# Kernel tuning notes

Measured on AMD Instinct MI355X. Metric: run time of the kernel, lower is better.

## Reference

```python
import jax, jax.numpy as jnp
import numpy as np

B, L, H, E = 4, 2048, 8, 64
S, D = L, E  # causal mask forces L == S


def setup_inputs() -> dict:
    key = jax.random.key(0)
    kq, kk, kv, km = jax.random.split(key, 4)
    return {
        "queries": jax.random.normal(kq, (B, L, H, E), dtype=jnp.float32),
        "keys": jax.random.normal(kk, (B, S, H, E), dtype=jnp.float32),
        "values": jax.random.normal(kv, (B, S, H, D), dtype=jnp.float32),
        "map": jax.random.normal(km, (S, S), dtype=jnp.float32),
    }


def reference(queries, keys, values, map):
    # queries: [B,L,H,E], keys: [B,S,H,E], values: [B,S,H,D], map: [S,S]
    E_ = queries.shape[-1]
    scale = 1.0 / jnp.sqrt(jnp.asarray(E_, dtype=queries.dtype))
    # raw attention scores: [B,H,L,S]
    scores = jnp.einsum("blhe,bshe->bhls", queries, keys)
    # mix scores with learned map along the key axis: [B,H,L,S]
    scores = jnp.einsum("bhls,st->bhlt", scores, map)
    # causal mask (TriangularCausalMask: triu with diagonal=1 is masked)
    Lq = queries.shape[1]
    causal = jnp.triu(jnp.ones((Lq, Lq), dtype=bool), k=1)  # [L,S]
    scores = jnp.where(causal[None, None, :, :], -jnp.inf, scores)
    attn = jax.nn.softmax(scale * scores, axis=-1)  # dropout p=0.0 -> identity
    out = jnp.einsum("bhls,bshd->blhd", attn, values)  # [B,L,H,D]
    return out
```

## Files before the change

kernel.cpp:

```cpp
#include <hip/hip_runtime.h>


typedef short bf16x8 __attribute__((ext_vector_type(8)));
typedef float f32x4 __attribute__((ext_vector_type(4)));
typedef float f32x16 __attribute__((ext_vector_type(16)));
typedef unsigned short u16x8 __attribute__((ext_vector_type(8)));
typedef unsigned int u32x4 __attribute__((ext_vector_type(4)));

typedef __attribute__((address_space(1))) const void gvoid;
typedef __attribute__((address_space(3))) void lvoid;

__device__ __forceinline__ unsigned short f2bf(float x) {
  unsigned int u = __float_as_uint(x);
  u += 0x7FFFu + ((u >> 16) & 1u);
  return (unsigned short)(u >> 16);
}
__device__ __forceinline__ float bf2f(unsigned short h) {
  return __uint_as_float(((unsigned int)h) << 16);
}
__device__ __forceinline__ unsigned int cvtpk(float lo, float hi) {
  unsigned int r;
  asm("v_cvt_pk_bf16_f32 %0, %1, %2" : "=v"(r) : "v"(lo), "v"(hi));
  return r;
}

__device__ __forceinline__ void gload16(const unsigned short* g, unsigned short* l) {
  __builtin_amdgcn_global_load_lds((gvoid*)g, (lvoid*)l, 16, 0, 0);
}

template <int NW>
__device__ __forceinline__ void stage_tile(const unsigned short* __restrict__ g,
                                           int gstride, unsigned short* l,
                                           int rows, int tid) {
  const int lane = tid & 63, w = tid >> 6;
  const int nch = rows << 3;
  for (int c0 = (w << 6); c0 < nch; c0 += NW * 64) {
    const int c = c0 + lane;
    const int row = c >> 3;
    const int bir = (c & 7) << 4;
    const int sb = bir ^ ((row & 7) << 4);
    gload16(g + (size_t)row * gstride + (sb >> 1), l + (size_t)c0 * 8);
  }
}

__device__ __forceinline__ int swz(int row, int byteInRow) {
  return row * 128 + (byteInRow ^ ((row & 7) << 4));
}

__global__ __launch_bounds__(256) void prep_m(const float* __restrict__ M,
                                              unsigned short* __restrict__ Mh,
                                              unsigned short* __restrict__ Ml) {
  __shared__ float Ts[64][68];
  const int s0 = blockIdx.x << 6, t0 = blockIdx.y << 6;
  const int tid = threadIdx.x, r = tid >> 2, c0 = (tid & 3) << 4;
  const float* src = M + (size_t)(s0 + r) * 2048 + t0 + c0;
#pragma unroll
  for (int j = 0; j < 4; ++j)
    *(float4*)&Ts[r][c0 + 4 * j] = *(const float4*)(src + 4 * j);
  __syncthreads();
  u16x8 h0, h1, l0v, l1v;
#pragma unroll
  for (int j = 0; j < 8; ++j) {
    float x = Ts[c0 + j][r];
    unsigned short hh = f2bf(x);
    h0[j] = hh; l0v[j] = f2bf(x - bf2f(hh));
  }
#pragma unroll
  for (int j = 8; j < 16; ++j) {
    float x = Ts[c0 + j][r];
    unsigned short hh = f2bf(x);
    h1[j - 8] = hh; l1v[j - 8] = f2bf(x - bf2f(hh));
  }
  const size_t o = (size_t)(t0 + r) * 2048 + s0 + c0;
  *(u16x8*)(Mh + o) = h0; *(u16x8*)(Mh + o + 8) = h1;
  *(u16x8*)(Ml + o) = l0v; *(u16x8*)(Ml + o + 8) = l1v;
}

__global__ __launch_bounds__(256) void prep_kv(const float* __restrict__ src4d,
                                               unsigned short* __restrict__ Dh,
                                               unsigned short* __restrict__ Dl,
                                               int has_lo) {
  __shared__ float Ts[64][68];
  const int s0 = blockIdx.x << 6, bh = blockIdx.y;
  const int b = bh >> 3, h = bh & 7;
  const int tid = threadIdx.x, r = tid >> 2, c0 = (tid & 3) << 4;
  const float* src = src4d + ((size_t)(b * 2048 + s0 + r) * 8 + h) * 64 + c0;
#pragma unroll
  for (int j = 0; j < 4; ++j)
    *(float4*)&Ts[r][c0 + 4 * j] = *(const float4*)(src + 4 * j);
  __syncthreads();
  u16x8 h0, h1, l0v, l1v;
#pragma unroll
  for (int j = 0; j < 8; ++j) {
    float x = Ts[c0 + j][r];
    unsigned short hh = f2bf(x);
    h0[j] = hh; l0v[j] = f2bf(x - bf2f(hh));
  }
#pragma unroll
  for (int j = 8; j < 16; ++j) {
    float x = Ts[c0 + j][r];
    unsigned short hh = f2bf(x);
    h1[j - 8] = hh; l1v[j - 8] = f2bf(x - bf2f(hh));
  }
  const size_t o = ((size_t)bh * 64 + r) * 2048 + s0 + c0;
  *(u16x8*)(Dh + o) = h0; *(u16x8*)(Dh + o + 8) = h1;
  if (has_lo) { *(u16x8*)(Dl + o) = l0v; *(u16x8*)(Dl + o + 8) = l1v; }
}

__global__ __launch_bounds__(512, 2) void km_mfma2(
    const unsigned short* __restrict__ Mth, const unsigned short* __restrict__ Mtl,
    const unsigned short* __restrict__ Kth, const unsigned short* __restrict__ Ktl,
    unsigned short* __restrict__ KMh, unsigned short* __restrict__ KMl) {
  __shared__ __attribute__((aligned(16))) unsigned short sm[40960];
  unsigned short* MH = sm;
  unsigned short* ML = sm + 16384;
  unsigned short* KH = sm + 32768;
  unsigned short* KL = sm + 36864;
  const int tid = threadIdx.x, lane = tid & 63, w = tid >> 6;
  const int g2 = lane >> 5, li5 = lane & 31;
  const int tc = w & 3, sh = w >> 2;

  const int x = (int)blockIdx.x & 7;
  const int bh = (int)blockIdx.x >> 3;
  const int t0 = x << 8;

  const unsigned short* MthB = Mth + (size_t)t0 * 2048;
  const unsigned short* MtlB = Mtl + (size_t)t0 * 2048;
  const unsigned short* KthB = Kth + (size_t)bh * 64 * 2048;
  const unsigned short* KtlB = Ktl + (size_t)bh * 64 * 2048;

  f32x16 acc[2][2];
#pragma unroll
  for (int tf = 0; tf < 2; ++tf)
#pragma unroll
    for (int ef = 0; ef < 2; ++ef)
      acc[tf][ef] = (f32x16){0,0,0,0,0,0,0,0,0,0,0,0,0,0,0,0};

  for (int s0 = 0; s0 < 2048; s0 += 64) {
    __syncthreads();
    stage_tile<8>(MthB + s0, 2048, MH, 256, tid);
    stage_tile<8>(MtlB + s0, 2048, ML, 256, tid);
    stage_tile<8>(KthB + s0, 2048, KH, 64, tid);
    stage_tile<8>(KtlB + s0, 2048, KL, 64, tid);
    asm volatile("s_waitcnt vmcnt(0)" ::: "memory");
    __syncthreads();

    __builtin_amdgcn_s_setprio(1);
#pragma unroll
    for (int kg = 0; kg < 2; ++kg) {
      const int kb = ((sh << 1) + kg) * 32 + (g2 << 4);
      const int ra0 = (tc << 6) + li5;
      const bf16x8 aH0 = *(const bf16x8*)((const char*)MH + swz(ra0, kb));
      const bf16x8 aL0 = *(const bf16x8*)((const char*)ML + swz(ra0, kb));
      const bf16x8 aH1 = *(const bf16x8*)((const char*)MH + swz(ra0 + 32, kb));
      const bf16x8 aL1 = *(const bf16x8*)((const char*)ML + swz(ra0 + 32, kb));
      const bf16x8 bH0 = *(const bf16x8*)((const char*)KH + swz(li5, kb));
      const bf16x8 bL0 = *(const bf16x8*)((const char*)KL + swz(li5, kb));
      const bf16x8 bH1 = *(const bf16x8*)((const char*)KH + swz(32 + li5, kb));
      const bf16x8 bL1 = *(const bf16x8*)((const char*)KL + swz(32 + li5, kb));
      acc[0][0] = __builtin_amdgcn_mfma_f32_32x32x16_bf16(aH0, bH0, acc[0][0], 0, 0, 0);
      acc[0][0] = __builtin_amdgcn_mfma_f32_32x32x16_bf16(aH0, bL0, acc[0][0], 0, 0, 0);
      acc[0][0] = __builtin_amdgcn_mfma_f32_32x32x16_bf16(aL0, bH0, acc[0][0], 0, 0, 0);
      acc[0][1] = __builtin_amdgcn_mfma_f32_32x32x16_bf16(aH0, bH1, acc[0][1], 0, 0, 0);
      acc[0][1] = __builtin_amdgcn_mfma_f32_32x32x16_bf16(aH0, bL1, acc[0][1], 0, 0, 0);
      acc[0][1] = __builtin_amdgcn_mfma_f32_32x32x16_bf16(aL0, bH1, acc[0][1], 0, 0, 0);
      acc[1][0] = __builtin_amdgcn_mfma_f32_32x32x16_bf16(aH1, bH0, acc[1][0], 0, 0, 0);
      acc[1][0] = __builtin_amdgcn_mfma_f32_32x32x16_bf16(aH1, bL0, acc[1][0], 0, 0, 0);
      acc[1][0] = __builtin_amdgcn_mfma_f32_32x32x16_bf16(aL1, bH0, acc[1][0], 0, 0, 0);
      acc[1][1] = __builtin_amdgcn_mfma_f32_32x32x16_bf16(aH1, bH1, acc[1][1], 0, 0, 0);
      acc[1][1] = __builtin_amdgcn_mfma_f32_32x32x16_bf16(aH1, bL1, acc[1][1], 0, 0, 0);
      acc[1][1] = __builtin_amdgcn_mfma_f32_32x32x16_bf16(aL1, bH1, acc[1][1], 0, 0, 0);
    }
    __builtin_amdgcn_s_setprio(0);
  }

  __syncthreads();
  float* red = (float*)sm;
  if (sh == 1) {
#pragma unroll
    for (int tf = 0; tf < 2; ++tf)
#pragma unroll
      for (int ef = 0; ef < 2; ++ef) {
        const int fi = (tc << 2) | (tf << 1) | ef;
        float* dst = red + (size_t)(fi * 64 + lane) * 17;
#pragma unroll
        for (int rr = 0; rr < 16; ++rr) dst[rr] = acc[tf][ef][rr];
      }
  }
  __syncthreads();
  if (sh == 0) {
    const size_t base = (size_t)bh * (2048 * 64);
#pragma unroll
    for (int tf = 0; tf < 2; ++tf)
#pragma unroll
      for (int ef = 0; ef < 2; ++ef) {
        const int fi = (tc << 2) | (tf << 1) | ef;
        const float* src = red + (size_t)(fi * 64 + lane) * 17;
#pragma unroll
        for (int rr = 0; rr < 16; ++rr) {
          const float v = acc[tf][ef][rr] + src[rr];
          const int trow = t0 + (tc << 6) + (tf << 5) + (g2 << 2) +
                           ((rr >> 2) << 3) + (rr & 3);
          const int e = (ef << 5) + li5;
          const unsigned short hh = f2bf(v);
          const size_t idx = base + (size_t)trow * 64 + e;
          KMh[idx] = hh;
          KMl[idx] = f2bf(v - bf2f(hh));
        }
      }
  }
}

__global__ __launch_bounds__(256, 3) void attn32(
    const float* __restrict__ Q, const unsigned short* __restrict__ KMh,
    const unsigned short* __restrict__ KMl, const unsigned short* __restrict__ Vt,
    float* __restrict__ Out, float* __restrict__ Opart, float* __restrict__ Ml) {
  __shared__ __attribute__((aligned(16))) unsigned short sm[24576];
  const int tid = threadIdx.x, lane = tid & 63, w = tid >> 6;
  const int g2 = lane >> 5, li5 = lane & 31;

  const int bid = (int)blockIdx.x;
  const int x = bid & 7, n = bid >> 3;
  const int slot = n >> 5, j = n & 31;
  const int bh = (x << 2) | (j & 3);
  const int kk = j >> 2;
  int lt, jt0, jtEnd;
  bool partial;
  if (slot == 2) {
    lt = kk; jt0 = 0; jtEnd = 2 * kk + 1; partial = false;
  } else {
    lt = 15 - kk;
    const int half = 16 - kk;
    jt0 = slot * half; jtEnd = jt0 + half - 1; partial = true;
  }
  const int b = bh >> 3, h = bh & 7;
  const int l0 = lt << 7;
  const int qg = l0 + (w << 5) + li5;
  const int rloc = (w << 5) + li5;

  const float SC2 = 0.18033688011112042f;
  bf16x8 qh[4], ql[4];
  {
    const float* qsrc = Q + (((size_t)(b * 2048 + qg) * 8 + h) << 6) + (g2 << 3);
#pragma unroll
    for (int kki = 0; kki < 4; ++kki) {
      const float4 v0 = *(const float4*)(qsrc + 16 * kki);
      const float4 v1 = *(const float4*)(qsrc + 16 * kki + 4);
      const float xs[8] = {v0.x, v0.y, v0.z, v0.w, v1.x, v1.y, v1.z, v1.w};
#pragma unroll
      for (int jj = 0; jj < 8; ++jj) {
        const float xv = xs[jj] * SC2;
        const unsigned short hh = f2bf(xv);
        qh[kki][jj] = (short)hh;
        ql[kki][jj] = (short)f2bf(xv - bf2f(hh));
      }
    }
  }

  f32x16 o0 = {0,0,0,0,0,0,0,0,0,0,0,0,0,0,0,0};
  f32x16 o1 = {0,0,0,0,0,0,0,0,0,0,0,0,0,0,0,0};
  f32x16 lsacc = {0,0,0,0,0,0,0,0,0,0,0,0,0,0,0,0};
  float m2 = -1e30f;
  bf16x8 ones;
#pragma unroll
  for (int jj = 0; jj < 8; ++jj) ones[jj] = (short)0x3F80;

  const unsigned short* KHb = KMh + (size_t)bh * 2048 * 64;
  const unsigned short* KLb = KMl + (size_t)bh * 2048 * 64;
  const unsigned short* VTb = Vt + (size_t)bh * 64 * 2048;

  const int jtmax_w = 2 * lt + (w >> 1);

  {
    unsigned short* s0b = sm + (jt0 & 1) * 12288;
    stage_tile<4>(KHb + (size_t)jt0 * 4096, 64, s0b, 64, tid);
    stage_tile<4>(KLb + (size_t)jt0 * 4096, 64, s0b + 4096, 64, tid);
    stage_tile<4>(VTb + jt0 * 64, 2048, s0b + 8192, 64, tid);
  }
  asm volatile("s_waitcnt vmcnt(0)" ::: "memory");
  __builtin_amdgcn_s_barrier();
  __builtin_amdgcn_sched_barrier(0);

  for (int jt = jt0; jt <= jtEnd; ++jt) {
    const int cur = jt & 1;
    if (jt < jtEnd) {
      unsigned short* nb = sm + (cur ^ 1) * 12288;
      stage_tile<4>(KHb + (size_t)(jt + 1) * 4096, 64, nb, 64, tid);
      stage_tile<4>(KLb + (size_t)(jt + 1) * 4096, 64, nb + 4096, 64, tid);
      stage_tile<4>(VTb + (jt + 1) * 64, 2048, nb + 8192, 64, tid);
    }

    if (jt <= jtmax_w) {
      const unsigned short* KH = sm + cur * 12288;
      const unsigned short* KL = KH + 4096;
      const unsigned short* VT = KH + 8192;

      f32x16 z0 = {0,0,0,0,0,0,0,0,0,0,0,0,0,0,0,0};
      f32x16 z1 = {0,0,0,0,0,0,0,0,0,0,0,0,0,0,0,0};
      __builtin_amdgcn_s_setprio(1);
#pragma unroll
      for (int kki = 0; kki < 4; ++kki) {
        const int cb = 32 * kki + 16 * g2;
        const bf16x8 a0h = *(const bf16x8*)((const char*)KH + swz(li5, cb));
        const bf16x8 a0l = *(const bf16x8*)((const char*)KL + swz(li5, cb));
        const bf16x8 a1h = *(const bf16x8*)((const char*)KH + swz(32 + li5, cb));
        const bf16x8 a1l = *(const bf16x8*)((const char*)KL + swz(32 + li5, cb));
        z0 = __builtin_amdgcn_mfma_f32_32x32x16_bf16(a0h, qh[kki], z0, 0, 0, 0);
        z0 = __builtin_amdgcn_mfma_f32_32x32x16_bf16(a0h, ql[kki], z0, 0, 0, 0);
        z0 = __builtin_amdgcn_mfma_f32_32x32x16_bf16(a0l, qh[kki], z0, 0, 0, 0);
        z1 = __builtin_amdgcn_mfma_f32_32x32x16_bf16(a1h, qh[kki], z1, 0, 0, 0);
        z1 = __builtin_amdgcn_mfma_f32_32x32x16_bf16(a1h, ql[kki], z1, 0, 0, 0);
        z1 = __builtin_amdgcn_mfma_f32_32x32x16_bf16(a1l, qh[kki], z1, 0, 0, 0);
      }
      __builtin_amdgcn_s_setprio(0);

      const bool needmask = (jt * 64 + 63 > l0 + (w << 5));
      if (needmask) {
        const int thr = qg - jt * 64;
#pragma unroll
        for (int rr = 0; rr < 16; ++rr) {
          const int tl = (g2 << 2) + ((rr >> 2) << 3) + (rr & 3);
          if (tl > thr) z0[rr] = -1e30f;
          if (tl + 32 > thr) z1[rr] = -1e30f;
        }
      }

      float t16[16];
#pragma unroll
      for (int rr = 0; rr < 16; ++rr) t16[rr] = fmaxf(z0[rr], z1[rr]);
#pragma unroll
      for (int s = 8; s; s >>= 1)
#pragma unroll
        for (int rr = 0; rr < 8; ++rr)
          if (rr < s) t16[rr] = fmaxf(t16[rr], t16[rr + s]);
      const float mx = fmaxf(t16[0], __shfl_xor(t16[0], 32));
      if (__any(mx > m2 + 11.0f)) {
        const float m2n = fmaxf(m2, mx);
        const float fs = exp2f(m2 - m2n);
        m2 = m2n;
#pragma unroll
        for (int rr = 0; rr < 16; ++rr) { o0[rr] *= fs; o1[rr] *= fs; }
        lsacc[0] *= fs;
      }

      float pv0[16], pv1[16];
#pragma unroll
      for (int rr = 0; rr < 16; ++rr) {
        pv0[rr] = exp2f(z0[rr] - m2);
        pv1[rr] = exp2f(z1[rr] - m2);
      }
      unsigned int W0[8], W1[8];
#pragma unroll
      for (int i = 0; i < 8; ++i) {
        W0[i] = cvtpk(pv0[2 * i], pv0[2 * i + 1]);
        W1[i] = cvtpk(pv1[2 * i], pv1[2 * i + 1]);
      }
      asm volatile("v_permlane32_swap_b32 %0, %1" : "+v"(W0[0]), "+v"(W0[2]));
      asm volatile("v_permlane32_swap_b32 %0, %1" : "+v"(W0[1]), "+v"(W0[3]));
      asm volatile("v_permlane32_swap_b32 %0, %1" : "+v"(W0[4]), "+v"(W0[6]));
      asm volatile("v_permlane32_swap_b32 %0, %1" : "+v"(W0[5]), "+v"(W0[7]));
      asm volatile("v_permlane32_swap_b32 %0, %1" : "+v"(W1[0]), "+v"(W1[2]));
      asm volatile("v_permlane32_swap_b32 %0, %1" : "+v"(W1[1]), "+v"(W1[3]));
      asm volatile("v_permlane32_swap_b32 %0, %1" : "+v"(W1[4]), "+v"(W1[6]));
      asm volatile("v_permlane32_swap_b32 %0, %1" : "+v"(W1[5]), "+v"(W1[7]));
      bf16x8 pf[4];
      {
        u32x4 f0 = {W0[0], W0[1], W0[2], W0[3]};
        u32x4 f1 = {W0[4], W0[5], W0[6], W0[7]};
        u32x4 f2 = {W1[0], W1[1], W1[2], W1[3]};
        u32x4 f3 = {W1[4], W1[5], W1[6], W1[7]};
        pf[0] = __builtin_bit_cast(bf16x8, f0);
        pf[1] = __builtin_bit_cast(bf16x8, f1);
        pf[2] = __builtin_bit_cast(bf16x8, f2);
        pf[3] = __builtin_bit_cast(bf16x8, f3);
      }

      __builtin_amdgcn_s_setprio(1);
#pragma unroll
      for (int kki = 0; kki < 4; ++kki) {
        const int cb = 32 * kki + 16 * g2;
        const bf16x8 v0f = *(const bf16x8*)((const char*)VT + swz(li5, cb));
        const bf16x8 v1f = *(const bf16x8*)((const char*)VT + swz(32 + li5, cb));
        o0 = __builtin_amdgcn_mfma_f32_32x32x16_bf16(v0f, pf[kki], o0, 0, 0, 0);
        o1 = __builtin_amdgcn_mfma_f32_32x32x16_bf16(v1f, pf[kki], o1, 0, 0, 0);
        lsacc = __builtin_amdgcn_mfma_f32_32x32x16_bf16(ones, pf[kki], lsacc, 0, 0, 0);
      }
      __builtin_amdgcn_s_setprio(0);
    }

    asm volatile("s_waitcnt vmcnt(0)" ::: "memory");
    __builtin_amdgcn_s_barrier();
    __builtin_amdgcn_sched_barrier(0);
  }

  if (!partial) {
    const float inv = 1.f / lsacc[0];
    float* ob = Out + (((size_t)(b * 2048 + qg) * 8 + h) << 6);
#pragma unroll
    for (int r2 = 0; r2 < 4; ++r2) {
      const int doff = (g2 << 2) + (r2 << 3);
      float4 s0 = make_float4(o0[4 * r2] * inv, o0[4 * r2 + 1] * inv,
                              o0[4 * r2 + 2] * inv, o0[4 * r2 + 3] * inv);
      *(float4*)(ob + doff) = s0;
      float4 s1 = make_float4(o1[4 * r2] * inv, o1[4 * r2 + 1] * inv,
                              o1[4 * r2 + 2] * inv, o1[4 * r2 + 3] * inv);
      *(float4*)(ob + 32 + doff) = s1;
    }
  } else {
    const size_t pidx = (((size_t)slot * 32 + bh) * 8 + kk) * 128 + rloc;
    float* op = Opart + pidx * 64;
#pragma unroll
    for (int r2 = 0; r2 < 4; ++r2) {
      const int doff = (g2 << 2) + (r2 << 3);
      *(float4*)(op + doff) =
          make_float4(o0[4 * r2], o0[4 * r2 + 1], o0[4 * r2 + 2], o0[4 * r2 + 3]);
      *(float4*)(op + 32 + doff) =
          make_float4(o1[4 * r2], o1[4 * r2 + 1], o1[4 * r2 + 2], o1[4 * r2 + 3]);
    }
    Ml[pidx * 2] = m2;
    Ml[pidx * 2 + 1] = lsacc[0];
  }
}

__global__ __launch_bounds__(256) void attn_combine(
    const float* __restrict__ Opart, const float* __restrict__ Ml,
    float* __restrict__ Out) {
  const int tid = threadIdx.x;
  const int rowg = (int)blockIdx.x * 32 + (tid >> 3);
  const int d0 = (tid & 7) << 3;
  const int r = rowg & 127, kk = (rowg >> 7) & 7, bh = rowg >> 10;
  const int b = bh >> 3, h = bh & 7;
  const int lt = 15 - kk;
  const size_t pidx = (((size_t)bh * 8 + kk) * 128 + r);
  const size_t PSLOT = (size_t)32 * 8 * 128 * 64;
  const size_t MSLOT = (size_t)32 * 8 * 128 * 2;
  const float m0 = Ml[pidx * 2], ls0 = Ml[pidx * 2 + 1];
  const float m1 = Ml[MSLOT + pidx * 2], ls1 = Ml[MSLOT + pidx * 2 + 1];
  const float mm = fmaxf(m0, m1);
  const float w0 = exp2f(m0 - mm), w1 = exp2f(m1 - mm);
  const float inv = 1.f / (ls0 * w0 + ls1 * w1);
  const float* p0 = Opart + pidx * 64 + d0;
  const float* p1 = Opart + PSLOT + pidx * 64 + d0;
  const float4 a0 = *(const float4*)(p0);
  const float4 a1 = *(const float4*)(p0 + 4);
  const float4 b0 = *(const float4*)(p1);
  const float4 b1 = *(const float4*)(p1 + 4);
  const int qg = lt * 128 + r;
  float* o = Out + (((size_t)(b * 2048 + qg) * 8 + h) << 6) + d0;
  *(float4*)o = make_float4((a0.x * w0 + b0.x * w1) * inv,
                            (a0.y * w0 + b0.y * w1) * inv,
                            (a0.z * w0 + b0.z * w1) * inv,
                            (a0.w * w0 + b0.w * w1) * inv);
  *(float4*)(o + 4) = make_float4((a1.x * w0 + b1.x * w1) * inv,
                                  (a1.y * w0 + b1.y * w1) * inv,
                                  (a1.z * w0 + b1.z * w1) * inv,
                                  (a1.w * w0 + b1.w * w1) * inv);
}

extern "C" void kernel_launch(void* const* d_in, const int* in_sizes, int n_in,
                              void* d_out, int out_size, void* d_ws, size_t ws_size,
                              hipStream_t stream) {
  const float* Q = (const float*)d_in[0];
  const float* K = (const float*)d_in[1];
  const float* V = (const float*)d_in[2];
  const float* M = (const float*)d_in[3];
  float* Out = (float*)d_out;
  char* ws = (char*)d_ws;
  const size_t MB = 1u << 20;
  unsigned short* Mth = (unsigned short*)(ws);
  unsigned short* Mtl = (unsigned short*)(ws + 8 * MB);
  unsigned short* Kth = (unsigned short*)(ws + 16 * MB);
  unsigned short* Ktl = (unsigned short*)(ws + 24 * MB);
  unsigned short* Vts = (unsigned short*)(ws + 32 * MB);
  unsigned short* KMh = (unsigned short*)(ws + 40 * MB);
  unsigned short* KMl = (unsigned short*)(ws + 48 * MB);
  float* Opart = (float*)(ws);
  float* Mlp = (float*)(ws + 16 * MB);

  prep_m<<<dim3(32, 32), 256, 0, stream>>>(M, Mth, Mtl);
  prep_kv<<<dim3(32, 32), 256, 0, stream>>>(K, Kth, Ktl, 1);
  prep_kv<<<dim3(32, 32), 256, 0, stream>>>(V, Vts, (unsigned short*)nullptr, 0);
  km_mfma2<<<dim3(256), 512, 0, stream>>>(Mth, Mtl, Kth, Ktl, KMh, KMl);
  attn32<<<dim3(768), 256, 0, stream>>>(Q, KMh, KMl, Vts, Out, Opart, Mlp);
  attn_combine<<<dim3(1024), 256, 0, stream>>>(Opart, Mlp, Out);
}
```

Measured before the change: 167.7 us.

## Replace split-K 32x32 KM GEMM with smaller-tile 16x16 MFMA kernel

Rewrites the K·map precompute kernel so each block covers 128 output rows with 256 threads and uses 16x16x32 MFMAs, instead of 256 rows with 512 threads split over K and reduced through shared memory. The grid doubles to 512 blocks and the shared-memory reduction step goes away. In exchange, each M and K tile loaded is reused across less work, and the final stores write 16 consecutive elements per row group rather than 32.

Result: faster. 147.9 us (-11.8%).

```diff
diff --git a/kernel.cpp b/kernel.cpp
--- a/kernel.cpp
+++ b/kernel.cpp
@@ -107,108 +107,76 @@
   if (has_lo) { *(u16x8*)(Dl + o) = l0v; *(u16x8*)(Dl + o + 8) = l1v; }
 }
 
-__global__ __launch_bounds__(512, 2) void km_mfma2(
+__global__ __launch_bounds__(256) void km_mfma(
     const unsigned short* __restrict__ Mth, const unsigned short* __restrict__ Mtl,
     const unsigned short* __restrict__ Kth, const unsigned short* __restrict__ Ktl,
     unsigned short* __restrict__ KMh, unsigned short* __restrict__ KMl) {
-  __shared__ __attribute__((aligned(16))) unsigned short sm[40960];
-  unsigned short* MH = sm;
-  unsigned short* ML = sm + 16384;
-  unsigned short* KH = sm + 32768;
-  unsigned short* KL = sm + 36864;
+  __shared__ __attribute__((aligned(16))) unsigned short sm[24576];
+  unsigned short* MtH = sm;
+  unsigned short* MtL = sm + 8192;
+  unsigned short* KtH = sm + 16384;
+  unsigned short* KtL = sm + 20480;
   const int tid = threadIdx.x, lane = tid & 63, w = tid >> 6;
-  const int g2 = lane >> 5, li5 = lane & 31;
-  const int tc = w & 3, sh = w >> 2;
-
-  const int x = (int)blockIdx.x & 7;
-  const int bh = (int)blockIdx.x >> 3;
-  const int t0 = x << 8;
-
-  const unsigned short* MthB = Mth + (size_t)t0 * 2048;
-  const unsigned short* MtlB = Mtl + (size_t)t0 * 2048;
-  const unsigned short* KthB = Kth + (size_t)bh * 64 * 2048;
-  const unsigned short* KtlB = Ktl + (size_t)bh * 64 * 2048;
-
-  f32x16 acc[2][2];
-#pragma unroll
-  for (int tf = 0; tf < 2; ++tf)
-#pragma unroll
-    for (int ef = 0; ef < 2; ++ef)
-      acc[tf][ef] = (f32x16){0,0,0,0,0,0,0,0,0,0,0,0,0,0,0,0};
+  const int g = lane >> 4, li = lane & 15;
+  const int t0 = blockIdx.x << 7;
+  const int bh = blockIdx.y;
+  const unsigned short* KtHb = Kth + (size_t)bh * 64 * 2048;
+  const unsigned short* KtLb = Ktl + (size_t)bh * 64 * 2048;
+
+  f32x4 acc[2][4];
+#pragma unroll
+  for (int mi = 0; mi < 2; ++mi)
+#pragma unroll
+    for (int ni = 0; ni < 4; ++ni) acc[mi][ni] = (f32x4){0.f, 0.f, 0.f, 0.f};
 
   for (int s0 = 0; s0 < 2048; s0 += 64) {
     __syncthreads();
-    stage_tile<8>(MthB + s0, 2048, MH, 256, tid);
-    stage_tile<8>(MtlB + s0, 2048, ML, 256, tid);
-    stage_tile<8>(KthB + s0, 2048, KH, 64, tid);
-    stage_tile<8>(KtlB + s0, 2048, KL, 64, tid);
+    stage_tile<4>(Mth + (size_t)t0 * 2048 + s0, 2048, MtH, 128, tid);
+    stage_tile<4>(Mtl + (size_t)t0 * 2048 + s0, 2048, MtL, 128, tid);
+    stage_tile<4>(KtHb + s0, 2048, KtH, 64, tid);
+    stage_tile<4>(KtLb + s0, 2048, KtL, 64, tid);
     asm volatile("s_waitcnt vmcnt(0)" ::: "memory");
     __syncthreads();
-
-    __builtin_amdgcn_s_setprio(1);
-#pragma unroll
-    for (int kg = 0; kg < 2; ++kg) {
-      const int kb = ((sh << 1) + kg) * 32 + (g2 << 4);
-      const int ra0 = (tc << 6) + li5;
-      const bf16x8 aH0 = *(const bf16x8*)((const char*)MH + swz(ra0, kb));
-      const bf16x8 aL0 = *(const bf16x8*)((const char*)ML + swz(ra0, kb));
-      const bf16x8 aH1 = *(const bf16x8*)((const char*)MH + swz(ra0 + 32, kb));
-      const bf16x8 aL1 = *(const bf16x8*)((const char*)ML + swz(ra0 + 32, kb));
-      const bf16x8 bH0 = *(const bf16x8*)((const char*)KH + swz(li5, kb));
-      const bf16x8 bL0 = *(const bf16x8*)((const char*)KL + swz(li5, kb));
-      const bf16x8 bH1 = *(const bf16x8*)((const char*)KH + swz(32 + li5, kb));
-      const bf16x8 bL1 = *(const bf16x8*)((const char*)KL + swz(32 + li5, kb));
-      acc[0][0] = __builtin_amdgcn_mfma_f32_32x32x16_bf16(aH0, bH0, acc[0][0], 0, 0, 0);
-      acc[0][0] = __builtin_amdgcn_mfma_f32_32x32x16_bf16(aH0, bL0, acc[0][0], 0, 0, 0);
-      acc[0][0] = __builtin_amdgcn_mfma_f32_32x32x16_bf16(aL0, bH0, acc[0][0], 0, 0, 0);
-      acc[0][1] = __builtin_amdgcn_mfma_f32_32x32x16_bf16(aH0, bH1, acc[0][1], 0, 0, 0);
-      acc[0][1] = __builtin_amdgcn_mfma_f32_32x32x16_bf16(aH0, bL1, acc[0][1], 0, 0, 0);
-      acc[0][1] = __builtin_amdgcn_mfma_f32_32x32x16_bf16(aL0, bH1, acc[0][1], 0, 0, 0);
-      acc[1][0] = __builtin_amdgcn_mfma_f32_32x32x16_bf16(aH1, bH0, acc[1][0], 0, 0, 0);
-      acc[1][0] = __builtin_amdgcn_mfma_f32_32x32x16_bf16(aH1, bL0, acc[1][0], 0, 0, 0);
-      acc[1][0] = __builtin_amdgcn_mfma_f32_32x32x16_bf16(aL1, bH0, acc[1][0], 0, 0, 0);
-      acc[1][1] = __builtin_amdgcn_mfma_f32_32x32x16_bf16(aH1, bH1, acc[1][1], 0, 0, 0);
-      acc[1][1] = __builtin_amdgcn_mfma_f32_32x32x16_bf16(aH1, bL1, acc[1][1], 0, 0, 0);
-      acc[1][1] = __builtin_amdgcn_mfma_f32_32x32x16_bf16(aL1, bH1, acc[1][1], 0, 0, 0);
-    }
-    __builtin_amdgcn_s_setprio(0);
-  }
-
-  __syncthreads();
-  float* red = (float*)sm;
-  if (sh == 1) {
-#pragma unroll
-    for (int tf = 0; tf < 2; ++tf)
-#pragma unroll
-      for (int ef = 0; ef < 2; ++ef) {
-        const int fi = (tc << 2) | (tf << 1) | ef;
-        float* dst = red + (size_t)(fi * 64 + lane) * 17;
-#pragma unroll
-        for (int rr = 0; rr < 16; ++rr) dst[rr] = acc[tf][ef][rr];
-      }
-  }
-  __syncthreads();
-  if (sh == 0) {
-    const size_t base = (size_t)bh * (2048 * 64);
-#pragma unroll
-    for (int tf = 0; tf < 2; ++tf)
-#pragma unroll
-      for (int ef = 0; ef < 2; ++ef) {
-        const int fi = (tc << 2) | (tf << 1) | ef;
-        const float* src = red + (size_t)(fi * 64 + lane) * 17;
-#pragma unroll
-        for (int rr = 0; rr < 16; ++rr) {
-          const float v = acc[tf][ef][rr] + src[rr];
-          const int trow = t0 + (tc << 6) + (tf << 5) + (g2 << 2) +
-                           ((rr >> 2) << 3) + (rr & 3);
-          const int e = (ef << 5) + li5;
-          const unsigned short hh = f2bf(v);
-          const size_t idx = base + (size_t)trow * 64 + e;
-          KMh[idx] = hh;
-          KMl[idx] = f2bf(v - bf2f(hh));
+#pragma unroll
+    for (int kk = 0; kk < 2; ++kk) {
+      const int kb = (kk * 32 + 8 * g) * 2;
+      bf16x8 aH[2], aL[2];
+#pragma unroll
+      for (int mi = 0; mi < 2; ++mi) {
+        const int row = (w << 5) + (mi << 4) + li;
+        aH[mi] = *(const bf16x8*)((const char*)MtH + swz(row, kb));
+        aL[mi] = *(const bf16x8*)((const char*)MtL + swz(row, kb));
+      }
+#pragma unroll
+      for (int ni = 0; ni < 4; ++ni) {
+        const int row = (ni << 4) + li;
+        const int off = swz(row, kb);
+        const bf16x8 bH = *(const bf16x8*)((const char*)KtH + off);
+        const bf16x8 bL = *(const bf16x8*)((const char*)KtL + off);
+#pragma unroll
+        for (int mi = 0; mi < 2; ++mi) {
+          acc[mi][ni] = __builtin_amdgcn_mfma_f32_16x16x32_bf16(aH[mi], bH, acc[mi][ni], 0, 0, 0);
+          acc[mi][ni] = __builtin_amdgcn_mfma_f32_16x16x32_bf16(aH[mi], bL, acc[mi][ni], 0, 0, 0);
+          acc[mi][ni] = __builtin_amdgcn_mfma_f32_16x16x32_bf16(aL[mi], bH, acc[mi][ni], 0, 0, 0);
         }
       }
-  }
+    }
+  }
+  const size_t base = (size_t)bh * 2048 * 64;
+#pragma unroll
+  for (int mi = 0; mi < 2; ++mi)
+#pragma unroll
+    for (int r = 0; r < 4; ++r) {
+      const int trow = t0 + (w << 5) + (mi << 4) + (g << 2) + r;
+#pragma unroll
+      for (int ni = 0; ni < 4; ++ni) {
+        const float x = acc[mi][ni][r];
+        const unsigned short hh = f2bf(x);
+        const size_t idx = base + (size_t)trow * 64 + (ni << 4) + li;
+        KMh[idx] = hh;
+        KMl[idx] = f2bf(x - bf2f(hh));
+      }
+    }
 }
 
 __global__ __launch_bounds__(256, 3) void attn32(
@@ -480,7 +448,7 @@
   prep_m<<<dim3(32, 32), 256, 0, stream>>>(M, Mth, Mtl);
   prep_kv<<<dim3(32, 32), 256, 0, stream>>>(K, Kth, Ktl, 1);
   prep_kv<<<dim3(32, 32), 256, 0, stream>>>(V, Vts, (unsigned short*)nullptr, 0);
-  km_mfma2<<<dim3(256), 512, 0, stream>>>(Mth, Mtl, Kth, Ktl, KMh, KMl);
+  km_mfma<<<dim3(16, 32), 256, 0, stream>>>(Mth, Mtl, Kth, Ktl, KMh, KMl);
   attn32<<<dim3(768), 256, 0, stream>>>(Q, KMh, KMl, Vts, Out, Opart, Mlp);
   attn_combine<<<dim3(1024), 256, 0, stream>>>(Opart, Mlp, Out);
 }
```
